# Optimization experiments

Measured on AMD Instinct MI355X. Metric: run time of the kernel, lower is better.

## Reference

```python
import jax, jax.numpy as jnp
import numpy as np

B, S1, S2, D1, D2, F = 8, 2048, 2048, 512, 512, 256

def setup_inputs() -> dict:
    key = jax.random.key(0)
    ks = jax.random.split(key, 10)
    sc1 = 1.0 / np.sqrt(D1)
    sc2 = 1.0 / np.sqrt(D2)
    scf = 1.0 / np.sqrt(F)
    return {
        "feat1": jax.random.normal(ks[0], (B, S1, D1), jnp.float32),
        "feat2": jax.random.normal(ks[1], (B, S2, D2), jnp.float32),
        "Wq": jax.random.normal(ks[2], (D1, F), jnp.float32) * sc1,
        "bq": jnp.zeros((F,), jnp.float32),
        "Wk": jax.random.normal(ks[3], (D2, F), jnp.float32) * sc2,
        "bk": jnp.zeros((F,), jnp.float32),
        "Wv": jax.random.normal(ks[4], (D2, F), jnp.float32) * sc2,
        "bv": jnp.zeros((F,), jnp.float32),
        "Wfc": jax.random.normal(ks[5], (F, F), jnp.float32) * scf,
        "bfc": jnp.zeros((F,), jnp.float32),
    }

def reference(feat1, feat2, Wq, bq, Wk, bk, Wv, bv, Wfc, bfc):
    Q = jnp.einsum('bsd,df->bsf', feat1, Wq) + bq          # [B,S1,F]
    K = jnp.einsum('btd,df->btf', feat2, Wk) + bk          # [B,S2,F]
    V = jnp.einsum('btd,df->btf', feat2, Wv) + bv          # [B,S2,F]
    scores = jnp.einsum('bsf,btf->bst', Q, K) / jnp.sqrt(jnp.float32(K.shape[-1]))
    attn = jax.nn.softmax(scores, axis=-1)                 # [B,S1,S2]
    attn_out = jnp.einsum('bst,btf->bsf', attn, V)         # [B,S1,F]
    out = jnp.einsum('bsf,fg->bsg', attn_out, Wfc) + bfc   # [B,S1,F]
    return out
```

## Files before the change

kernel.cpp:

```cpp
#include <hip/hip_runtime.h>
#include <hip/hip_bf16.h>

#define B_ 8
#define S1_ 2048
#define S2_ 2048
#define D_ 512
#define F_ 256

typedef __attribute__((ext_vector_type(4))) float f32x4;
typedef __attribute__((ext_vector_type(8))) short s16x8;
typedef __attribute__((ext_vector_type(4))) short s16x4;

__device__ __forceinline__ short f2bf(float x) {
  union { float f; unsigned u; } v; v.f = x;
  unsigned r = v.u + 0x7fffu + ((v.u >> 16) & 1u);
  return (short)(r >> 16);
}

__device__ __forceinline__ int pk2bf(float a, float b) {
  union { __hip_bfloat162 h; int i; } u;
  u.h = __float22bfloat162_rn(make_float2(a, b));
  return u.i;
}

__global__ __launch_bounds__(256) void wtrans_kernel(
    const float* __restrict__ Wq, const float* __restrict__ Wk,
    const float* __restrict__ Wv, const float* __restrict__ Wfc,
    short* __restrict__ Wqt, short* __restrict__ Wkt,
    short* __restrict__ Wvt, short* __restrict__ Wfct) {
  int y = blockIdx.y;
  const float* W; short* Wt; int D;
  if (y == 0)      { W = Wq;  Wt = Wqt;  D = 512; }
  else if (y == 1) { W = Wk;  Wt = Wkt;  D = 512; }
  else if (y == 2) { W = Wv;  Wt = Wvt;  D = 512; }
  else             { W = Wfc; Wt = Wfct; D = 256; }
  int tiles_d = D >> 6;
  int bx = blockIdx.x;
  if (bx >= tiles_d * 4) return;
  int d0 = (bx % tiles_d) * 64, f0 = (bx / tiles_d) * 64;

  __shared__ short Ts[64][68];
  int t = threadIdx.x;
  int r = t >> 2, c16 = (t & 3) * 16;
  {
    const float* src = W + (size_t)(d0 + r) * F_ + f0 + c16;
    f32x4 v0 = *(const f32x4*)(src);
    f32x4 v1 = *(const f32x4*)(src + 4);
    f32x4 v2 = *(const f32x4*)(src + 8);
    f32x4 v3 = *(const f32x4*)(src + 12);
    s16x8 s0, s1;
    ((int*)&s0)[0] = pk2bf(v0[0], v0[1]); ((int*)&s0)[1] = pk2bf(v0[2], v0[3]);
    ((int*)&s0)[2] = pk2bf(v1[0], v1[1]); ((int*)&s0)[3] = pk2bf(v1[2], v1[3]);
    ((int*)&s1)[0] = pk2bf(v2[0], v2[1]); ((int*)&s1)[1] = pk2bf(v2[2], v2[3]);
    ((int*)&s1)[2] = pk2bf(v3[0], v3[1]); ((int*)&s1)[3] = pk2bf(v3[2], v3[3]);
    *(s16x8*)(&Ts[r][c16]) = s0;
    *(s16x8*)(&Ts[r][c16 + 8]) = s1;
  }
  __syncthreads();
  {
    int fr = t >> 2, dc16 = (t & 3) * 16;
    s16x8 o0, o1;
    for (int j = 0; j < 8; ++j) o0[j] = Ts[dc16 + j][fr];
    for (int j = 0; j < 8; ++j) o1[j] = Ts[dc16 + 8 + j][fr];
    short* dst = Wt + (size_t)(f0 + fr) * D + d0 + dc16;
    *(s16x8*)dst = o0;
    *(s16x8*)(dst + 8) = o1;
  }
}

__global__ __launch_bounds__(256, 3) void proj_kernel(
    const float* __restrict__ feat1, const float* __restrict__ feat2,
    const short* __restrict__ Wqt, const short* __restrict__ Wkt,
    const short* __restrict__ Wvt,
    const float* __restrict__ bq, const float* __restrict__ bk,
    const float* __restrict__ bv,
    short* __restrict__ Qw, short* __restrict__ Kw, short* __restrict__ Vtw) {
  const float* A; const short* Wt; const float* bias; short* outp;
  float scale; int trans;
  if (blockIdx.y == 0)      { A = feat1; Wt = Wqt; bias = bq; outp = Qw;  scale = 0.0625f; trans = 0; }
  else if (blockIdx.y == 1) { A = feat2; Wt = Wkt; bias = bk; outp = Kw;  scale = 1.0f;    trans = 0; }
  else                      { A = feat2; Wt = Wvt; bias = bv; outp = Vtw; scale = 1.0f;    trans = 1; }

  __shared__ __align__(16) short As[64][72];
  __shared__ __align__(16) short Ws[256][72];

  int m0 = blockIdx.x * 64;
  int t = threadIdx.x;
  int w = t >> 6, L = t & 63, rowA = L & 15, quad = L >> 4;
  int ar = t >> 2, ac16 = (t & 3) * 16;

  f32x4 acc[4][4];
  for (int i = 0; i < 4; ++i)
    for (int j = 0; j < 4; ++j) acc[i][j] = (f32x4){0.f, 0.f, 0.f, 0.f};

  for (int k0 = 0; k0 < D_; k0 += 64) {
    {
      const float* src = A + (size_t)(m0 + ar) * D_ + k0 + ac16;
      f32x4 v0 = *(const f32x4*)(src);
      f32x4 v1 = *(const f32x4*)(src + 4);
      f32x4 v2 = *(const f32x4*)(src + 8);
      f32x4 v3 = *(const f32x4*)(src + 12);
      s16x8 s0, s1;
      ((int*)&s0)[0] = pk2bf(v0[0], v0[1]); ((int*)&s0)[1] = pk2bf(v0[2], v0[3]);
      ((int*)&s0)[2] = pk2bf(v1[0], v1[1]); ((int*)&s0)[3] = pk2bf(v1[2], v1[3]);
      ((int*)&s1)[0] = pk2bf(v2[0], v2[1]); ((int*)&s1)[1] = pk2bf(v2[2], v2[3]);
      ((int*)&s1)[2] = pk2bf(v3[0], v3[1]); ((int*)&s1)[3] = pk2bf(v3[2], v3[3]);
      *(s16x8*)(&As[ar][ac16]) = s0;
      *(s16x8*)(&As[ar][ac16 + 8]) = s1;
    }
    for (int p = 0; p < 4; ++p) {
      int r = (t >> 2) + p * 64;
      const short* src = Wt + (size_t)r * D_ + k0 + ac16;
      *(s16x8*)(&Ws[r][ac16]) = *(const s16x8*)(src);
      *(s16x8*)(&Ws[r][ac16 + 8]) = *(const s16x8*)(src + 8);
    }
    __syncthreads();
    for (int kt = 0; kt < 2; ++kt) {
      s16x8 a[4];
      for (int mt = 0; mt < 4; ++mt)
        a[mt] = *(const s16x8*)(&As[mt * 16 + rowA][kt * 32 + quad * 8]);
      for (int nt = 0; nt < 4; ++nt) {
        s16x8 bfr = *(const s16x8*)(&Ws[w * 64 + nt * 16 + rowA][kt * 32 + quad * 8]);
        for (int mt = 0; mt < 4; ++mt)
          acc[mt][nt] = __builtin_amdgcn_mfma_f32_16x16x32_bf16(a[mt], bfr, acc[mt][nt], 0, 0, 0);
      }
    }
    __syncthreads();
  }

  if (!trans) {
    float bn[4];
    for (int nt = 0; nt < 4; ++nt) bn[nt] = bias[w * 64 + nt * 16 + rowA];
    for (int mt = 0; mt < 4; ++mt) {
      int m = m0 + mt * 16 + quad * 4;
      for (int nt = 0; nt < 4; ++nt) {
        int n = w * 64 + nt * 16 + rowA;
        for (int r = 0; r < 4; ++r)
          outp[(size_t)(m + r) * F_ + n] = f2bf((acc[mt][nt][r] + bn[nt]) * scale);
      }
    }
  } else {
    int bb = m0 >> 11;
    int tbase = m0 & (S2_ - 1);
    float bn[4];
    for (int nt = 0; nt < 4; ++nt) bn[nt] = bias[w * 64 + nt * 16 + rowA];
    for (int nt = 0; nt < 4; ++nt) {
      int f = w * 64 + nt * 16 + rowA;
      for (int mt = 0; mt < 4; ++mt) {
        int tt = tbase + mt * 16 + quad * 4;
        s16x4 o;
        for (int r = 0; r < 4; ++r) o[r] = f2bf(acc[mt][nt][r] + bn[nt]);
        *(s16x4*)(outp + ((size_t)bb * F_ + f) * S2_ + tt) = o;
      }
    }
  }
}

__global__ __launch_bounds__(512, 2) void flash_kernel(
    const short* __restrict__ Q,
    const short* __restrict__ K,
    const short* __restrict__ Vt,
    short* __restrict__ O) {
  __shared__ __align__(16) short Ks[2][64][264];
  __shared__ __align__(16) short Vs[2][256][72];
  __shared__ __align__(16) short Ps[2][64][72];

  int b = blockIdx.x & 7;
  int s0 = (blockIdx.x >> 3) * 64;
  int t = threadIdx.x;
  int w = t >> 6, L = t & 63, rowA = L & 15, quad = L >> 4;
  int isS = (w < 4);

  const short* Kb = K + (size_t)b * S2_ * F_;
  const short* Vb = Vt + (size_t)b * F_ * S2_;

  int kr = t >> 5, kc8 = (t & 31) * 8;
  int vr = t >> 3, vc8 = (t & 7) * 8;

  int rs = (w & 1) * 32, cs = ((w >> 1) & 1) * 32;
  int mg = (w - 4) & 1, fg = ((w - 4) >> 1) & 1;

  s16x8 qf[2][8];
  if (isS) {
    const short* Qb = Q + ((size_t)b * S1_ + s0 + rs) * F_;
    for (int mt = 0; mt < 2; ++mt)
      for (int kt = 0; kt < 8; ++kt)
        qf[mt][kt] = *(const s16x8*)(Qb + (size_t)(mt * 16 + rowA) * F_ + kt * 32 + quad * 8);
  }
  f32x4 o[2][8];
  for (int i = 0; i < 2; ++i)
    for (int j = 0; j < 8; ++j) o[i][j] = (f32x4){0.f, 0.f, 0.f, 0.f};
  float l_lane[2][4] = {{0.f,0.f,0.f,0.f},{0.f,0.f,0.f,0.f}};

  s16x8 kpre[4], vpre[4];
  for (int p = 0; p < 4; ++p)
    kpre[p] = *(const s16x8*)(Kb + (size_t)(kr + p * 16) * F_ + kc8);
  for (int p = 0; p < 4; ++p)
    *(s16x8*)(&Ks[0][kr + p * 16][kc8]) = kpre[p];
  for (int p = 0; p < 4; ++p)
    kpre[p] = *(const s16x8*)(Kb + (size_t)(64 + kr + p * 16) * F_ + kc8);
  for (int p = 0; p < 4; ++p)
    vpre[p] = *(const s16x8*)(Vb + (size_t)(vr + p * 64) * S2_ + vc8);

  for (int it = 0; it <= 32; ++it) {
    int cb = it & 1;
    __syncthreads();
    if (it < 32) {
      for (int p = 0; p < 4; ++p)
        *(s16x8*)(&Vs[cb][vr + p * 64][vc8]) = vpre[p];
      if (it < 31) {
        for (int p = 0; p < 4; ++p)
          *(s16x8*)(&Ks[1 - cb][kr + p * 16][kc8]) = kpre[p];
        int n0 = (it + 1) * 64;
        for (int p = 0; p < 4; ++p)
          vpre[p] = *(const s16x8*)(Vb + (size_t)(vr + p * 64) * S2_ + n0 + vc8);
      }
      if (it < 30) {
        int n0 = (it + 2) * 64;
        for (int p = 0; p < 4; ++p)
          kpre[p] = *(const s16x8*)(Kb + (size_t)(n0 + kr + p * 16) * F_ + kc8);
      }
    }
    if (isS) {
      if (it < 32) {
        f32x4 s[2][2];
        for (int i = 0; i < 2; ++i)
          for (int j = 0; j < 2; ++j) s[i][j] = (f32x4){0.f, 0.f, 0.f, 0.f};
        for (int kt = 0; kt < 8; ++kt) {
          s16x8 bf0 = *(const s16x8*)(&Ks[cb][cs + rowA][kt * 32 + quad * 8]);
          s16x8 bf1 = *(const s16x8*)(&Ks[cb][cs + 16 + rowA][kt * 32 + quad * 8]);
          for (int mt = 0; mt < 2; ++mt) {
            s[mt][0] = __builtin_amdgcn_mfma_f32_16x16x32_bf16(qf[mt][kt], bf0, s[mt][0], 0, 0, 0);
            s[mt][1] = __builtin_amdgcn_mfma_f32_16x16x32_bf16(qf[mt][kt], bf1, s[mt][1], 0, 0, 0);
          }
        }
        for (int mt = 0; mt < 2; ++mt)
          for (int nt = 0; nt < 2; ++nt)
            for (int r = 0; r < 4; ++r) {
              float p = __expf(s[mt][nt][r]);
              l_lane[mt][r] += p;
              Ps[cb][rs + mt * 16 + quad * 4 + r][cs + nt * 16 + rowA] = f2bf(p);
            }
      }
    } else {
      if (it > 0) {
        int pb = 1 - cb;
        s16x8 pa[2][2];
        for (int mt = 0; mt < 2; ++mt)
          for (int kt = 0; kt < 2; ++kt)
            pa[mt][kt] = *(const s16x8*)(&Ps[pb][mg * 32 + mt * 16 + rowA][kt * 32 + quad * 8]);
        for (int ft = 0; ft < 8; ++ft)
          for (int kt = 0; kt < 2; ++kt) {
            s16x8 vf = *(const s16x8*)(&Vs[pb][fg * 128 + ft * 16 + rowA][kt * 32 + quad * 8]);
            for (int mt = 0; mt < 2; ++mt)
              o[mt][ft] = __builtin_amdgcn_mfma_f32_16x16x32_bf16(pa[mt][kt], vf, o[mt][ft], 0, 0, 0);
          }
      }
    }
  }

  float* lf = (float*)&Ks[0][0][0];
  if (isS) {
    for (int mt = 0; mt < 2; ++mt)
      for (int r = 0; r < 4; ++r) {
        float x = l_lane[mt][r];
        for (int off = 1; off < 16; off <<= 1)
          x += __shfl_xor(x, off, 64);
        if (rowA == 0)
          lf[((w >> 1) & 1) * 64 + rs + mt * 16 + quad * 4 + r] = x;
      }
  }
  __syncthreads();
  if (!isS) {
    short* Ob = O + ((size_t)b * S1_ + s0) * F_;
    for (int mt = 0; mt < 2; ++mt)
      for (int r = 0; r < 4; ++r) {
        int row = mg * 32 + mt * 16 + quad * 4 + r;
        float inv = 1.0f / (lf[row] + lf[64 + row]);
        for (int ft = 0; ft < 8; ++ft)
          Ob[(size_t)row * F_ + fg * 128 + ft * 16 + rowA] = f2bf(o[mt][ft][r] * inv);
      }
  }
}

__global__ __launch_bounds__(256) void fc_kernel(
    const short* __restrict__ AO,
    const short* __restrict__ Wt,
    const float* __restrict__ bias,
    float* __restrict__ out) {
  __shared__ __align__(16) short As[64][72];
  __shared__ __align__(16) short Ws[128][72];

  int m0 = blockIdx.x * 64;
  int n0 = blockIdx.y * 128;
  int t = threadIdx.x;
  int w = t >> 6, L = t & 63, rowA = L & 15, quad = L >> 4;
  int wy = w & 1, wx = w >> 1;

  int ar = t >> 2, ac16 = (t & 3) * 16;
  int wr = t >> 1, wc32 = (t & 1) * 32;

  s16x8 apre[2], wpre[4];
  {
    const short* asrc = AO + (size_t)(m0 + ar) * F_ + ac16;
    apre[0] = *(const s16x8*)(asrc);
    apre[1] = *(const s16x8*)(asrc + 8);
    const short* wsrc = Wt + (size_t)(n0 + wr) * F_ + wc32;
    for (int j = 0; j < 4; ++j) wpre[j] = *(const s16x8*)(wsrc + j * 8);
  }

  f32x4 acc[2][4];
  for (int i = 0; i < 2; ++i)
    for (int j = 0; j < 4; ++j) acc[i][j] = (f32x4){0.f, 0.f, 0.f, 0.f};

  for (int k0 = 0; k0 < F_; k0 += 64) {
    *(s16x8*)(&As[ar][ac16]) = apre[0];
    *(s16x8*)(&As[ar][ac16 + 8]) = apre[1];
    for (int j = 0; j < 4; ++j) *(s16x8*)(&Ws[wr][wc32 + j * 8]) = wpre[j];
    __syncthreads();
    if (k0 + 64 < F_) {
      const short* asrc = AO + (size_t)(m0 + ar) * F_ + k0 + 64 + ac16;
      apre[0] = *(const s16x8*)(asrc);
      apre[1] = *(const s16x8*)(asrc + 8);
      const short* wsrc = Wt + (size_t)(n0 + wr) * F_ + k0 + 64 + wc32;
      for (int j = 0; j < 4; ++j) wpre[j] = *(const s16x8*)(wsrc + j * 8);
    }
    for (int kt = 0; kt < 2; ++kt) {
      s16x8 a[2];
      for (int mt = 0; mt < 2; ++mt)
        a[mt] = *(const s16x8*)(&As[wy * 32 + mt * 16 + rowA][kt * 32 + quad * 8]);
      for (int nt = 0; nt < 4; ++nt) {
        s16x8 bfr = *(const s16x8*)(&Ws[wx * 64 + nt * 16 + rowA][kt * 32 + quad * 8]);
        for (int mt = 0; mt < 2; ++mt)
          acc[mt][nt] = __builtin_amdgcn_mfma_f32_16x16x32_bf16(a[mt], bfr, acc[mt][nt], 0, 0, 0);
      }
    }
    __syncthreads();
  }

  float bn[4];
  for (int nt = 0; nt < 4; ++nt) bn[nt] = bias[n0 + wx * 64 + nt * 16 + rowA];
  for (int mt = 0; mt < 2; ++mt) {
    int m = m0 + wy * 32 + mt * 16 + quad * 4;
    for (int nt = 0; nt < 4; ++nt) {
      int n = n0 + wx * 64 + nt * 16 + rowA;
      for (int r = 0; r < 4; ++r)
        out[(size_t)(m + r) * F_ + n] = acc[mt][nt][r] + bn[nt];
    }
  }
}

extern "C" void kernel_launch(void* const* d_in, const int* in_sizes, int n_in,
                              void* d_out, int out_size, void* d_ws, size_t ws_size,
                              hipStream_t stream) {
  const float* feat1 = (const float*)d_in[0];
  const float* feat2 = (const float*)d_in[1];
  const float* Wq  = (const float*)d_in[2];
  const float* bq  = (const float*)d_in[3];
  const float* Wk  = (const float*)d_in[4];
  const float* bk  = (const float*)d_in[5];
  const float* Wv  = (const float*)d_in[6];
  const float* bv  = (const float*)d_in[7];
  const float* Wfc = (const float*)d_in[8];
  const float* bfc = (const float*)d_in[9];
  float* out = (float*)d_out;
  char* ws = (char*)d_ws;

  short* Qw   = (short*)(ws);
  short* Kw   = (short*)(ws + (size_t)(8u  << 20));
  short* Vtw  = (short*)(ws + (size_t)(16u << 20));
  short* AOw  = (short*)(ws + (size_t)(24u << 20));
  short* Wqt  = (short*)(ws + (size_t)(32u << 20));
  short* Wkt  = Wqt + 256 * 512;
  short* Wvt  = Wkt + 256 * 512;
  short* Wfct = Wvt + 256 * 512;

  wtrans_kernel<<<dim3(32, 4), 256, 0, stream>>>(Wq, Wk, Wv, Wfc, Wqt, Wkt, Wvt, Wfct);
  proj_kernel<<<dim3(256, 3), 256, 0, stream>>>(feat1, feat2, Wqt, Wkt, Wvt,
                                                bq, bk, bv, Qw, Kw, Vtw);
  flash_kernel<<<dim3(256), 512, 0, stream>>>(Qw, Kw, Vtw, AOw);
  fc_kernel<<<dim3(256, 2), 256, 0, stream>>>(AOw, Wfct, bfc, out);
}
```

Before: 188.7 us.

## Fuse FC projection into flash kernel and use direct global-to-LDS swizzled loads

The output FC GEMM is folded into the flash attention kernel's epilogue. The normalized attention output is staged in LDS and multiplied by the bf16 Wfc directly, which removes the intermediate AO buffer round-trip and one kernel launch. K/V tiles are now loaded with global_load_lds into unpadded, XOR-swizzled LDS, replacing the register-staged prefetch. The PV warps are remapped so each covers all 64 rows and a 64-column F slice. The fused epilogue reads Wfc from global memory per block, and the grid is only 256 blocks.

```diff
diff --git a/kernel.cpp b/kernel.cpp
--- a/kernel.cpp
+++ b/kernel.cpp
@@ -21,6 +21,12 @@
   union { __hip_bfloat162 h; int i; } u;
   u.h = __float22bfloat162_rn(make_float2(a, b));
   return u.i;
+}
+
+__device__ __forceinline__ void gll16(const short* g, short* l) {
+  __builtin_amdgcn_global_load_lds(
+      (const __attribute__((address_space(1))) void*)g,
+      (__attribute__((address_space(3))) void*)l, 16, 0, 0);
 }
 
 __global__ __launch_bounds__(256) void wtrans_kernel(
@@ -160,10 +166,13 @@
     const short* __restrict__ Q,
     const short* __restrict__ K,
     const short* __restrict__ Vt,
-    short* __restrict__ O) {
-  __shared__ __align__(16) short Ks[2][64][264];
-  __shared__ __align__(16) short Vs[2][256][72];
+    const short* __restrict__ Wfct,
+    const float* __restrict__ bfc,
+    float* __restrict__ out) {
+  __shared__ __align__(16) short Ks[2][64][256];
+  __shared__ __align__(16) short Vs[2][256][64];
   __shared__ __align__(16) short Ps[2][64][72];
+  __shared__ float lf[128];
 
   int b = blockIdx.x & 7;
   int s0 = (blockIdx.x >> 3) * 64;
@@ -174,11 +183,8 @@
   const short* Kb = K + (size_t)b * S2_ * F_;
   const short* Vb = Vt + (size_t)b * F_ * S2_;
 
-  int kr = t >> 5, kc8 = (t & 31) * 8;
-  int vr = t >> 3, vc8 = (t & 7) * 8;
-
   int rs = (w & 1) * 32, cs = ((w >> 1) & 1) * 32;
-  int mg = (w - 4) & 1, fg = ((w - 4) >> 1) & 1;
+  int kxor = (rowA & 7) << 4;
 
   s16x8 qf[2][8];
   if (isS) {
@@ -187,38 +193,42 @@
       for (int kt = 0; kt < 8; ++kt)
         qf[mt][kt] = *(const s16x8*)(Qb + (size_t)(mt * 16 + rowA) * F_ + kt * 32 + quad * 8);
   }
-  f32x4 o[2][8];
-  for (int i = 0; i < 2; ++i)
-    for (int j = 0; j < 8; ++j) o[i][j] = (f32x4){0.f, 0.f, 0.f, 0.f};
+  f32x4 o[4][4];
+  for (int i = 0; i < 4; ++i)
+    for (int j = 0; j < 4; ++j) o[i][j] = (f32x4){0.f, 0.f, 0.f, 0.f};
   float l_lane[2][4] = {{0.f,0.f,0.f,0.f},{0.f,0.f,0.f,0.f}};
 
-  s16x8 kpre[4], vpre[4];
-  for (int p = 0; p < 4; ++p)
-    kpre[p] = *(const s16x8*)(Kb + (size_t)(kr + p * 16) * F_ + kc8);
-  for (int p = 0; p < 4; ++p)
-    *(s16x8*)(&Ks[0][kr + p * 16][kc8]) = kpre[p];
-  for (int p = 0; p < 4; ++p)
-    kpre[p] = *(const s16x8*)(Kb + (size_t)(64 + kr + p * 16) * F_ + kc8);
-  for (int p = 0; p < 4; ++p)
-    vpre[p] = *(const s16x8*)(Vb + (size_t)(vr + p * 64) * S2_ + vc8);
+  {
+    int vL5 = L >> 5, vc = L & 31;
+#pragma unroll
+    for (int j = 0; j < 4; ++j) {
+      int row = 8 * w + 2 * j + vL5;
+      const short* src = Kb + (size_t)row * F_ + ((vc ^ (row & 7)) << 3);
+      gll16(src, &Ks[0][8 * w + 2 * j][0]);
+    }
+  }
 
   for (int it = 0; it <= 32; ++it) {
     int cb = it & 1;
     __syncthreads();
     if (it < 32) {
-      for (int p = 0; p < 4; ++p)
-        *(s16x8*)(&Vs[cb][vr + p * 64][vc8]) = vpre[p];
+      int vn0 = it << 6;
+      int vL3 = L >> 3, vxor = ((L & 7) ^ ((L >> 3) & 7)) << 3;
+#pragma unroll
+      for (int j = 0; j < 4; ++j) {
+        int row = 32 * w + 8 * j + vL3;
+        const short* src = Vb + (size_t)row * S2_ + vn0 + vxor;
+        gll16(src, &Vs[cb][32 * w + 8 * j][0]);
+      }
       if (it < 31) {
-        for (int p = 0; p < 4; ++p)
-          *(s16x8*)(&Ks[1 - cb][kr + p * 16][kc8]) = kpre[p];
-        int n0 = (it + 1) * 64;
-        for (int p = 0; p < 4; ++p)
-          vpre[p] = *(const s16x8*)(Vb + (size_t)(vr + p * 64) * S2_ + n0 + vc8);
-      }
-      if (it < 30) {
-        int n0 = (it + 2) * 64;
-        for (int p = 0; p < 4; ++p)
-          kpre[p] = *(const s16x8*)(Kb + (size_t)(n0 + kr + p * 16) * F_ + kc8);
+        int kn0 = (it + 1) << 6;
+        int kL5 = L >> 5, kc = L & 31;
+#pragma unroll
+        for (int j = 0; j < 4; ++j) {
+          int row = 8 * w + 2 * j + kL5;
+          const short* src = Kb + (size_t)(kn0 + row) * F_ + ((kc ^ (row & 7)) << 3);
+          gll16(src, &Ks[1 - cb][8 * w + 2 * j][0]);
+        }
       }
     }
     if (isS) {
@@ -226,9 +236,13 @@
         f32x4 s[2][2];
         for (int i = 0; i < 2; ++i)
           for (int j = 0; j < 2; ++j) s[i][j] = (f32x4){0.f, 0.f, 0.f, 0.f};
+        const char* kb0 = (const char*)&Ks[cb][0][0] + ((size_t)(cs + rowA) << 9);
+        const char* kb1 = kb0 + (16 << 9);
+#pragma unroll
         for (int kt = 0; kt < 8; ++kt) {
-          s16x8 bf0 = *(const s16x8*)(&Ks[cb][cs + rowA][kt * 32 + quad * 8]);
-          s16x8 bf1 = *(const s16x8*)(&Ks[cb][cs + 16 + rowA][kt * 32 + quad * 8]);
+          int off = (kt * 64 + quad * 16) ^ kxor;
+          s16x8 bf0 = *(const s16x8*)(kb0 + off);
+          s16x8 bf1 = *(const s16x8*)(kb1 + off);
           for (int mt = 0; mt < 2; ++mt) {
             s[mt][0] = __builtin_amdgcn_mfma_f32_16x16x32_bf16(qf[mt][kt], bf0, s[mt][0], 0, 0, 0);
             s[mt][1] = __builtin_amdgcn_mfma_f32_16x16x32_bf16(qf[mt][kt], bf1, s[mt][1], 0, 0, 0);
@@ -245,21 +259,24 @@
     } else {
       if (it > 0) {
         int pb = 1 - cb;
-        s16x8 pa[2][2];
-        for (int mt = 0; mt < 2; ++mt)
+        s16x8 pa[4][2];
+#pragma unroll
+        for (int mt = 0; mt < 4; ++mt)
           for (int kt = 0; kt < 2; ++kt)
-            pa[mt][kt] = *(const s16x8*)(&Ps[pb][mg * 32 + mt * 16 + rowA][kt * 32 + quad * 8]);
-        for (int ft = 0; ft < 8; ++ft)
+            pa[mt][kt] = *(const s16x8*)(&Ps[pb][mt * 16 + rowA][kt * 32 + quad * 8]);
+        const char* vb0 = (const char*)&Vs[pb][0][0] + (size_t)((w - 4) * 64 + rowA) * 128;
+#pragma unroll
+        for (int ft = 0; ft < 4; ++ft)
           for (int kt = 0; kt < 2; ++kt) {
-            s16x8 vf = *(const s16x8*)(&Vs[pb][fg * 128 + ft * 16 + rowA][kt * 32 + quad * 8]);
-            for (int mt = 0; mt < 2; ++mt)
+            int off = (kt * 64 + quad * 16) ^ kxor;
+            s16x8 vf = *(const s16x8*)(vb0 + (size_t)(ft * 16) * 128 + off);
+            for (int mt = 0; mt < 4; ++mt)
               o[mt][ft] = __builtin_amdgcn_mfma_f32_16x16x32_bf16(pa[mt][kt], vf, o[mt][ft], 0, 0, 0);
           }
       }
     }
   }
 
-  float* lf = (float*)&Ks[0][0][0];
   if (isS) {
     for (int mt = 0; mt < 2; ++mt)
       for (int r = 0; r < 4; ++r) {
@@ -271,82 +288,41 @@
       }
   }
   __syncthreads();
+
+  short (*Olds)[264] = (short (*)[264])(&Ks[0][0][0]);
   if (!isS) {
-    short* Ob = O + ((size_t)b * S1_ + s0) * F_;
-    for (int mt = 0; mt < 2; ++mt)
+    int fgc = (w - 4) * 64;
+    for (int mt = 0; mt < 4; ++mt)
       for (int r = 0; r < 4; ++r) {
-        int row = mg * 32 + mt * 16 + quad * 4 + r;
+        int row = mt * 16 + quad * 4 + r;
         float inv = 1.0f / (lf[row] + lf[64 + row]);
-        for (int ft = 0; ft < 8; ++ft)
-          Ob[(size_t)row * F_ + fg * 128 + ft * 16 + rowA] = f2bf(o[mt][ft][r] * inv);
-      }
-  }
-}
-
-__global__ __launch_bounds__(256) void fc_kernel(
-    const short* __restrict__ AO,
-    const short* __restrict__ Wt,
-    const float* __restrict__ bias,
-    float* __restrict__ out) {
-  __shared__ __align__(16) short As[64][72];
-  __shared__ __align__(16) short Ws[128][72];
-
-  int m0 = blockIdx.x * 64;
-  int n0 = blockIdx.y * 128;
-  int t = threadIdx.x;
-  int w = t >> 6, L = t & 63, rowA = L & 15, quad = L >> 4;
-  int wy = w & 1, wx = w >> 1;
-
-  int ar = t >> 2, ac16 = (t & 3) * 16;
-  int wr = t >> 1, wc32 = (t & 1) * 32;
-
-  s16x8 apre[2], wpre[4];
-  {
-    const short* asrc = AO + (size_t)(m0 + ar) * F_ + ac16;
-    apre[0] = *(const s16x8*)(asrc);
-    apre[1] = *(const s16x8*)(asrc + 8);
-    const short* wsrc = Wt + (size_t)(n0 + wr) * F_ + wc32;
-    for (int j = 0; j < 4; ++j) wpre[j] = *(const s16x8*)(wsrc + j * 8);
-  }
-
-  f32x4 acc[2][4];
-  for (int i = 0; i < 2; ++i)
-    for (int j = 0; j < 4; ++j) acc[i][j] = (f32x4){0.f, 0.f, 0.f, 0.f};
-
-  for (int k0 = 0; k0 < F_; k0 += 64) {
-    *(s16x8*)(&As[ar][ac16]) = apre[0];
-    *(s16x8*)(&As[ar][ac16 + 8]) = apre[1];
-    for (int j = 0; j < 4; ++j) *(s16x8*)(&Ws[wr][wc32 + j * 8]) = wpre[j];
-    __syncthreads();
-    if (k0 + 64 < F_) {
-      const short* asrc = AO + (size_t)(m0 + ar) * F_ + k0 + 64 + ac16;
-      apre[0] = *(const s16x8*)(asrc);
-      apre[1] = *(const s16x8*)(asrc + 8);
-      const short* wsrc = Wt + (size_t)(n0 + wr) * F_ + k0 + 64 + wc32;
-      for (int j = 0; j < 4; ++j) wpre[j] = *(const s16x8*)(wsrc + j * 8);
-    }
-    for (int kt = 0; kt < 2; ++kt) {
-      s16x8 a[2];
-      for (int mt = 0; mt < 2; ++mt)
-        a[mt] = *(const s16x8*)(&As[wy * 32 + mt * 16 + rowA][kt * 32 + quad * 8]);
-      for (int nt = 0; nt < 4; ++nt) {
-        s16x8 bfr = *(const s16x8*)(&Ws[wx * 64 + nt * 16 + rowA][kt * 32 + quad * 8]);
-        for (int mt = 0; mt < 2; ++mt)
-          acc[mt][nt] = __builtin_amdgcn_mfma_f32_16x16x32_bf16(a[mt], bfr, acc[mt][nt], 0, 0, 0);
-      }
-    }
-    __syncthreads();
-  }
-
-  float bn[4];
-  for (int nt = 0; nt < 4; ++nt) bn[nt] = bias[n0 + wx * 64 + nt * 16 + rowA];
-  for (int mt = 0; mt < 2; ++mt) {
-    int m = m0 + wy * 32 + mt * 16 + quad * 4;
-    for (int nt = 0; nt < 4; ++nt) {
-      int n = n0 + wx * 64 + nt * 16 + rowA;
-      for (int r = 0; r < 4; ++r)
-        out[(size_t)(m + r) * F_ + n] = acc[mt][nt][r] + bn[nt];
-    }
+        for (int ft = 0; ft < 4; ++ft)
+          Olds[row][fgc + ft * 16 + rowA] = f2bf(o[mt][ft][r] * inv);
+      }
+  }
+  __syncthreads();
+
+  int mrow = (w & 3) * 16;
+  int ng = (w >> 2) * 128;
+  f32x4 fc[8];
+  for (int i = 0; i < 8; ++i) fc[i] = (f32x4){0.f, 0.f, 0.f, 0.f};
+#pragma unroll
+  for (int kt = 0; kt < 8; ++kt) {
+    s16x8 a = *(const s16x8*)(&Olds[mrow + rowA][kt * 32 + quad * 8]);
+#pragma unroll
+    for (int nt = 0; nt < 8; ++nt) {
+      s16x8 bfr = *(const s16x8*)(Wfct + (size_t)(ng + nt * 16 + rowA) * 256 + kt * 32 + quad * 8);
+      fc[nt] = __builtin_amdgcn_mfma_f32_16x16x32_bf16(a, bfr, fc[nt], 0, 0, 0);
+    }
+  }
+  float* Ob = out + ((size_t)b * S1_ + s0) * F_;
+#pragma unroll
+  for (int nt = 0; nt < 8; ++nt) {
+    int g = ng + nt * 16 + rowA;
+    float bias = bfc[g];
+#pragma unroll
+    for (int r = 0; r < 4; ++r)
+      Ob[(size_t)(mrow + quad * 4 + r) * F_ + g] = fc[nt][r] + bias;
   }
 }
 
@@ -369,7 +345,6 @@
   short* Qw   = (short*)(ws);
   short* Kw   = (short*)(ws + (size_t)(8u  << 20));
   short* Vtw  = (short*)(ws + (size_t)(16u << 20));
-  short* AOw  = (short*)(ws + (size_t)(24u << 20));
   short* Wqt  = (short*)(ws + (size_t)(32u << 20));
   short* Wkt  = Wqt + 256 * 512;
   short* Wvt  = Wkt + 256 * 512;
@@ -378,6 +353,5 @@
   wtrans_kernel<<<dim3(32, 4), 256, 0, stream>>>(Wq, Wk, Wv, Wfc, Wqt, Wkt, Wvt, Wfct);
   proj_kernel<<<dim3(256, 3), 256, 0, stream>>>(feat1, feat2, Wqt, Wkt, Wvt,
                                                 bq, bk, bv, Qw, Kw, Vtw);
-  flash_kernel<<<dim3(256), 512, 0, stream>>>(Qw, Kw, Vtw, AOw);
-  fc_kernel<<<dim3(256, 2), 256, 0, stream>>>(AOw, Wfct, bfc, out);
-}
+  flash_kernel<<<dim3(256), 512, 0, stream>>>(Qw, Kw, Vtw, Wfct, bfc, out);
+}
```

New measurement: 200.9 us. 6.5% more time.

## Double-buffer projection LDS tiles with register prefetch of next K slice

Applied to the files above, without the earlier changes.

Rewrites the projection GEMM main loop to use a K step of 32 with two LDS buffers. The next slice of activations and weights is prefetched into registers while the MFMAs run on the current buffer, which also drops the trailing barrier per iteration. The aim is to hide global-load latency in the Q/K/V projection, at the cost of more iterations and extra registers for the prefetch.

```diff
diff --git a/kernel.cpp b/kernel.cpp
--- a/kernel.cpp
+++ b/kernel.cpp
@@ -81,51 +81,55 @@
   else if (blockIdx.y == 1) { A = feat2; Wt = Wkt; bias = bk; outp = Kw;  scale = 1.0f;    trans = 0; }
   else                      { A = feat2; Wt = Wvt; bias = bv; outp = Vtw; scale = 1.0f;    trans = 1; }
 
-  __shared__ __align__(16) short As[64][72];
-  __shared__ __align__(16) short Ws[256][72];
+  __shared__ __align__(16) short As[2][64][40];
+  __shared__ __align__(16) short Ws[2][256][40];
 
   int m0 = blockIdx.x * 64;
   int t = threadIdx.x;
   int w = t >> 6, L = t & 63, rowA = L & 15, quad = L >> 4;
-  int ar = t >> 2, ac16 = (t & 3) * 16;
+  int sr = t >> 2, sc8 = (t & 3) * 8;
 
   f32x4 acc[4][4];
   for (int i = 0; i < 4; ++i)
     for (int j = 0; j < 4; ++j) acc[i][j] = (f32x4){0.f, 0.f, 0.f, 0.f};
 
-  for (int k0 = 0; k0 < D_; k0 += 64) {
+  f32x4 a0, a1;
+  s16x8 wp[4];
+  {
+    const float* src = A + (size_t)(m0 + sr) * D_ + sc8;
+    a0 = *(const f32x4*)(src);
+    a1 = *(const f32x4*)(src + 4);
+    for (int p = 0; p < 4; ++p)
+      wp[p] = *(const s16x8*)(Wt + (size_t)(sr + p * 64) * D_ + sc8);
+  }
+
+  for (int k = 0; k < 16; ++k) {
+    int cur = k & 1;
     {
-      const float* src = A + (size_t)(m0 + ar) * D_ + k0 + ac16;
-      f32x4 v0 = *(const f32x4*)(src);
-      f32x4 v1 = *(const f32x4*)(src + 4);
-      f32x4 v2 = *(const f32x4*)(src + 8);
-      f32x4 v3 = *(const f32x4*)(src + 12);
-      s16x8 s0, s1;
-      ((int*)&s0)[0] = pk2bf(v0[0], v0[1]); ((int*)&s0)[1] = pk2bf(v0[2], v0[3]);
-      ((int*)&s0)[2] = pk2bf(v1[0], v1[1]); ((int*)&s0)[3] = pk2bf(v1[2], v1[3]);
-      ((int*)&s1)[0] = pk2bf(v2[0], v2[1]); ((int*)&s1)[1] = pk2bf(v2[2], v2[3]);
-      ((int*)&s1)[2] = pk2bf(v3[0], v3[1]); ((int*)&s1)[3] = pk2bf(v3[2], v3[3]);
-      *(s16x8*)(&As[ar][ac16]) = s0;
-      *(s16x8*)(&As[ar][ac16 + 8]) = s1;
-    }
-    for (int p = 0; p < 4; ++p) {
-      int r = (t >> 2) + p * 64;
-      const short* src = Wt + (size_t)r * D_ + k0 + ac16;
-      *(s16x8*)(&Ws[r][ac16]) = *(const s16x8*)(src);
-      *(s16x8*)(&Ws[r][ac16 + 8]) = *(const s16x8*)(src + 8);
+      s16x8 s;
+      ((int*)&s)[0] = pk2bf(a0[0], a0[1]); ((int*)&s)[1] = pk2bf(a0[2], a0[3]);
+      ((int*)&s)[2] = pk2bf(a1[0], a1[1]); ((int*)&s)[3] = pk2bf(a1[2], a1[3]);
+      *(s16x8*)(&As[cur][sr][sc8]) = s;
+      for (int p = 0; p < 4; ++p)
+        *(s16x8*)(&Ws[cur][sr + p * 64][sc8]) = wp[p];
     }
     __syncthreads();
-    for (int kt = 0; kt < 2; ++kt) {
-      s16x8 a[4];
+    if (k < 15) {
+      int k0 = (k + 1) * 32;
+      const float* src = A + (size_t)(m0 + sr) * D_ + k0 + sc8;
+      a0 = *(const f32x4*)(src);
+      a1 = *(const f32x4*)(src + 4);
+      for (int p = 0; p < 4; ++p)
+        wp[p] = *(const s16x8*)(Wt + (size_t)(sr + p * 64) * D_ + k0 + sc8);
+    }
+    s16x8 a[4];
+    for (int mt = 0; mt < 4; ++mt)
+      a[mt] = *(const s16x8*)(&As[cur][mt * 16 + rowA][quad * 8]);
+    for (int nt = 0; nt < 4; ++nt) {
+      s16x8 bfr = *(const s16x8*)(&Ws[cur][w * 64 + nt * 16 + rowA][quad * 8]);
       for (int mt = 0; mt < 4; ++mt)
-        a[mt] = *(const s16x8*)(&As[mt * 16 + rowA][kt * 32 + quad * 8]);
-      for (int nt = 0; nt < 4; ++nt) {
-        s16x8 bfr = *(const s16x8*)(&Ws[w * 64 + nt * 16 + rowA][kt * 32 + quad * 8]);
-        for (int mt = 0; mt < 4; ++mt)
-          acc[mt][nt] = __builtin_amdgcn_mfma_f32_16x16x32_bf16(a[mt], bfr, acc[mt][nt], 0, 0, 0);
-      }
-    }
-    __syncthreads();
+        acc[mt][nt] = __builtin_amdgcn_mfma_f32_16x16x32_bf16(a[mt], bfr, acc[mt][nt], 0, 0, 0);
+    }
   }
 
   if (!trans) {
```

Measured after the change: 192.5 us. 1.02x slower.
